# Optimization experiments

Measured on AMD Instinct MI355X. Metric: run time of the kernel, lower is better.

The kernel has to match this reference:

```python
import jax, jax.numpy as jnp
import numpy as np

DIM = 1024
NUM_HEADS = 16
B, T = 2, 2048


def setup_inputs() -> dict:
    key = jax.random.key(0)
    ks = jax.random.split(key, 7)
    s = 0.02
    return {
        "Q": jax.random.normal(ks[0], (B, T, DIM), dtype=jnp.float32),
        "K": jax.random.normal(ks[1], (B, T, DIM), dtype=jnp.float32),
        "V": jax.random.normal(ks[2], (B, T, DIM), dtype=jnp.float32),
        "Wq": jax.random.normal(ks[3], (DIM, DIM), dtype=jnp.float32) * s,
        "Wk": jax.random.normal(ks[4], (DIM, DIM), dtype=jnp.float32) * s,
        "Wv": jax.random.normal(ks[5], (DIM, DIM), dtype=jnp.float32) * s,
        "Wp": jax.random.normal(ks[6], (DIM, DIM), dtype=jnp.float32) * s,
    }


def _split_heads(x, h):
    b, t, d = x.shape
    return x.reshape(b, t, h, d // h).transpose(0, 2, 1, 3)  # b h t d


def reference(Q, K, V, Wq, Wk, Wv, Wp):
    b, t, d = Q.shape
    h = NUM_HEADS
    # NOTE: module scales by 1/sqrt(dim) (full model dim), not 1/sqrt(head_dim)
    scale = 1.0 / np.sqrt(d).astype(np.float32)
    # torch Linear: x @ W.T (bias=False)
    q = _split_heads(Q @ Wq.T, h)  # b h t hd
    k = _split_heads(K @ Wk.T, h)
    v = _split_heads(V @ Wv.T, h)
    att = jnp.einsum('bhid,bhjd->bhij', q, k) * scale  # b h t t
    causal = jnp.tril(jnp.ones((t, t), dtype=bool))
    att = jnp.where(causal[None, None], att, -jnp.inf)
    att = jax.nn.softmax(att, axis=-1)
    y = jnp.einsum('bhij,bhjd->bhid', att, v)  # b h t hd
    y = y.transpose(0, 2, 1, 3).reshape(b, t, d)
    y = y @ Wp.T
    return (y, att, k, v)
```

## Files before the change

kernel.cpp:

```cpp
#include <hip/hip_runtime.h>

typedef __attribute__((ext_vector_type(8))) short s16x8;
typedef __attribute__((ext_vector_type(4))) float f32x4;

static __device__ __forceinline__ unsigned short f2bf(float f) {
  union { float f; unsigned int u; } v; v.f = f;
  unsigned int u = v.u;
  u += 0x7fffu + ((u >> 16) & 1u);
  return (unsigned short)(u >> 16);
}
static __device__ __forceinline__ void gload16(const void* g, void* l) {
  __builtin_amdgcn_global_load_lds((const __attribute__((address_space(1))) unsigned int*)g,
                                   (__attribute__((address_space(3))) unsigned int*)l, 16, 0, 0);
}

__global__ __launch_bounds__(256) void cast7_bf16(
    const float* __restrict__ i0, const float* __restrict__ i1, const float* __restrict__ i2,
    const float* __restrict__ i3, const float* __restrict__ i4, const float* __restrict__ i5,
    const float* __restrict__ i6,
    unsigned short* __restrict__ o0, unsigned short* __restrict__ o1,
    unsigned short* __restrict__ o2, unsigned short* __restrict__ o3,
    unsigned short* __restrict__ o4, unsigned short* __restrict__ o5,
    unsigned short* __restrict__ o6) {
  const int z = blockIdx.z;
  const float* in = z == 0 ? i0 : z == 1 ? i1 : z == 2 ? i2 : z == 3 ? i3 : z == 4 ? i4
                    : z == 5 ? i5 : i6;
  unsigned short* out = z == 0 ? o0 : z == 1 ? o1 : z == 2 ? o2 : z == 3 ? o3 : z == 4 ? o4
                        : z == 5 ? o5 : o6;
  const int n = (z < 3) ? 4194304 : 1048576;
  int i = (blockIdx.x * 256 + threadIdx.x) * 8;
  if (i >= n) return;
  float4 a = *reinterpret_cast<const float4*>(in + i);
  float4 b = *reinterpret_cast<const float4*>(in + i + 4);
  s16x8 o;
  o[0] = (short)f2bf(a.x); o[1] = (short)f2bf(a.y);
  o[2] = (short)f2bf(a.z); o[3] = (short)f2bf(a.w);
  o[4] = (short)f2bf(b.x); o[5] = (short)f2bf(b.y);
  o[6] = (short)f2bf(b.z); o[7] = (short)f2bf(b.w);
  *reinterpret_cast<s16x8*>(out + i) = o;
}

__global__ __launch_bounds__(256) void gemm_bf16(
    const unsigned short* __restrict__ A0, const unsigned short* __restrict__ A1,
    const unsigned short* __restrict__ A2,
    const unsigned short* __restrict__ W0, const unsigned short* __restrict__ W1,
    const unsigned short* __restrict__ W2,
    unsigned short* __restrict__ Oq, unsigned short* __restrict__ Ok,
    float* __restrict__ Kf, unsigned short* __restrict__ OvT,
    float* __restrict__ Vf) {
  __shared__ __align__(16) char LDS[32768];

  const int z = blockIdx.z;
  const unsigned short* A = z == 0 ? A0 : z == 1 ? A1 : A2;
  const unsigned short* W = z == 0 ? W0 : z == 1 ? W1 : W2;

  const int tid = threadIdx.x, lane = tid & 63, w = tid >> 6;
  const int wm = w >> 1, wn = w & 1;
  const int row0 = blockIdx.y * 128, col0 = blockIdx.x * 128;

  f32x4 acc[4][4];
#pragma unroll
  for (int m = 0; m < 4; ++m)
#pragma unroll
    for (int n = 0; n < 4; ++n) acc[m][n] = f32x4{0.f, 0.f, 0.f, 0.f};

  const int srow = tid >> 3;
  const int swb = ((tid & 7) * 16) ^ ((srow & 7) << 4);
  const unsigned short* aSrc = A + (size_t)(row0 + srow) * 1024 + (swb >> 1);
  const unsigned short* bSrc = W + (size_t)(col0 + srow) * 1024 + (swb >> 1);
  char* ldsA = LDS + w * 1024;
  char* ldsB = LDS + 16384 + w * 1024;

  const int lr = lane & 15, g16 = (lane >> 4) * 16;

  for (int k0 = 0; k0 < 1024; k0 += 64) {
    __syncthreads();
#pragma unroll
    for (int p = 0; p < 4; ++p) gload16(aSrc + (size_t)p * 32 * 1024 + k0, ldsA + p * 4096);
#pragma unroll
    for (int p = 0; p < 4; ++p) gload16(bSrc + (size_t)p * 32 * 1024 + k0, ldsB + p * 4096);
    __syncthreads();

    s16x8 af[2][4], bf[2][4];
#pragma unroll
    for (int ks = 0; ks < 2; ++ks) {
#pragma unroll
      for (int m = 0; m < 4; ++m) {
        int r = wm * 64 + m * 16 + lr;
        int cb = (ks * 64 + g16) ^ ((r & 7) << 4);
        af[ks][m] = *reinterpret_cast<const s16x8*>(LDS + r * 128 + cb);
      }
#pragma unroll
      for (int n = 0; n < 4; ++n) {
        int r = wn * 64 + n * 16 + lr;
        int cb = (ks * 64 + g16) ^ ((r & 7) << 4);
        bf[ks][n] = *reinterpret_cast<const s16x8*>(LDS + 16384 + r * 128 + cb);
      }
    }
#pragma unroll
    for (int ks = 0; ks < 2; ++ks)
#pragma unroll
      for (int m = 0; m < 4; ++m)
#pragma unroll
        for (int n = 0; n < 4; ++n)
          acc[m][n] = __builtin_amdgcn_mfma_f32_16x16x32_bf16(af[ks][m], bf[ks][n], acc[m][n], 0, 0, 0);
  }

  const int er = (lane >> 4) * 4, ec = lane & 15;
  const int b = row0 >> 11, trow = row0 & 2047;

  {
    float* F = (z == 1) ? Kf : (z == 2) ? Vf : nullptr;
    if (F) {
#pragma unroll
      for (int m = 0; m < 4; ++m)
#pragma unroll
        for (int n = 0; n < 4; ++n)
#pragma unroll
          for (int j = 0; j < 4; ++j) {
            int t = trow + wm * 64 + m * 16 + er + j;
            int gd = col0 + wn * 64 + n * 16 + ec;
            F[((size_t)(b * 16 + (gd >> 6)) * 2048 + t) * 64 + (gd & 63)] = acc[m][n][j];
          }
    }
  }

  __syncthreads();
  if (z == 2) {
#pragma unroll
    for (int m = 0; m < 4; ++m)
#pragma unroll
      for (int n = 0; n < 4; ++n)
#pragma unroll
        for (int j = 0; j < 4; ++j) {
          int d = wn * 64 + n * 16 + ec, t = wm * 64 + m * 16 + er + j;
          *reinterpret_cast<short*>(LDS + d * 256 + t * 2) = (short)f2bf(acc[m][n][j]);
        }
    __syncthreads();
    const int dr = tid >> 1, half = tid & 1;
    const int gd = col0 + dr, h = gd >> 6, dd = gd & 63;
    unsigned short* dst = OvT + ((size_t)(b * 16 + h) * 64 + dd) * 2048 + trow + half * 64;
    const char* src = LDS + dr * 256 + half * 128;
#pragma unroll
    for (int i = 0; i < 8; ++i)
      *reinterpret_cast<s16x8*>(dst + i * 8) = *reinterpret_cast<const s16x8*>(src + i * 16);
  } else {
    unsigned short* On = (z == 0) ? Oq : Ok;
#pragma unroll
    for (int m = 0; m < 4; ++m)
#pragma unroll
      for (int n = 0; n < 4; ++n)
#pragma unroll
        for (int j = 0; j < 4; ++j) {
          int r = wm * 64 + m * 16 + er + j, c = wn * 64 + n * 16 + ec;
          *reinterpret_cast<short*>(LDS + r * 256 + c * 2) = (short)f2bf(acc[m][n][j]);
        }
    __syncthreads();
    const int r = tid >> 1, half = tid & 1;
    const int h = (col0 >> 6) + half;
    unsigned short* dst = On + ((size_t)(b * 16 + h) * 2048 + trow + r) * 64;
    const char* src = LDS + r * 256 + half * 128;
#pragma unroll
    for (int i = 0; i < 8; ++i)
      *reinterpret_cast<s16x8*>(dst + i * 8) = *reinterpret_cast<const s16x8*>(src + i * 16);
  }
}

__global__ __launch_bounds__(256) void gemm_proj64(
    const unsigned short* __restrict__ A, const unsigned short* __restrict__ W,
    float* __restrict__ Orm) {
  __shared__ __align__(16) char LDS[24576];

  const int tid = threadIdx.x, lane = tid & 63, w = tid >> 6;
  const int row0 = blockIdx.y * 64, col0 = blockIdx.x * 128;

  f32x4 acc[4][2];
#pragma unroll
  for (int m = 0; m < 4; ++m)
#pragma unroll
    for (int n = 0; n < 2; ++n) acc[m][n] = f32x4{0.f, 0.f, 0.f, 0.f};

  const int srow = tid >> 3;
  const int swb = ((tid & 7) * 16) ^ ((srow & 7) << 4);
  const unsigned short* aSrc = A + (size_t)(row0 + srow) * 1024 + (swb >> 1);
  const unsigned short* bSrc = W + (size_t)(col0 + srow) * 1024 + (swb >> 1);
  char* ldsA = LDS + w * 1024;
  char* ldsB = LDS + 8192 + w * 1024;

  const int lr = lane & 15, g16 = (lane >> 4) * 16;

  for (int k0 = 0; k0 < 1024; k0 += 64) {
    __syncthreads();
#pragma unroll
    for (int p = 0; p < 2; ++p) gload16(aSrc + (size_t)p * 32 * 1024 + k0, ldsA + p * 4096);
#pragma unroll
    for (int p = 0; p < 4; ++p) gload16(bSrc + (size_t)p * 32 * 1024 + k0, ldsB + p * 4096);
    __syncthreads();

    s16x8 af[2][4], bf[2][2];
#pragma unroll
    for (int ks = 0; ks < 2; ++ks) {
#pragma unroll
      for (int m = 0; m < 4; ++m) {
        int r = m * 16 + lr;
        int cb = (ks * 64 + g16) ^ ((r & 7) << 4);
        af[ks][m] = *reinterpret_cast<const s16x8*>(LDS + r * 128 + cb);
      }
#pragma unroll
      for (int n = 0; n < 2; ++n) {
        int r = w * 32 + n * 16 + lr;
        int cb = (ks * 64 + g16) ^ ((r & 7) << 4);
        bf[ks][n] = *reinterpret_cast<const s16x8*>(LDS + 8192 + r * 128 + cb);
      }
    }
#pragma unroll
    for (int ks = 0; ks < 2; ++ks)
#pragma unroll
      for (int m = 0; m < 4; ++m)
#pragma unroll
        for (int n = 0; n < 2; ++n)
          acc[m][n] = __builtin_amdgcn_mfma_f32_16x16x32_bf16(af[ks][m], bf[ks][n], acc[m][n], 0, 0, 0);
  }

  const int er = (lane >> 4) * 4, ec = lane & 15;
#pragma unroll
  for (int m = 0; m < 4; ++m)
#pragma unroll
    for (int n = 0; n < 2; ++n)
#pragma unroll
      for (int j = 0; j < 4; ++j)
        Orm[(size_t)(row0 + m * 16 + er + j) * 1024 + col0 + w * 32 + n * 16 + ec] = acc[m][n][j];
}

#define ALD 68

__global__ __launch_bounds__(256) void attn_kernel(
    const unsigned short* __restrict__ qw, const unsigned short* __restrict__ kw,
    const unsigned short* __restrict__ vt, float* __restrict__ att_out,
    unsigned short* __restrict__ yb) {
  __shared__ __align__(16) char LDSA[2][16384];
  __shared__ short Pl[4][16 * ALD];

  const int tid = threadIdx.x, lane = tid & 63, w = tid >> 6;
  const int flat = blockIdx.y * 32 + blockIdx.x;
  const int xcd = flat & 7, idx = flat >> 3;
  const int bh = xcd * 4 + (idx >> 5);
  const int iblk = 31 - (idx & 31);
  const float scale2 = 0.03125f * 1.44269504f;

  const int lr = lane & 15, g16 = (lane >> 4) * 16;
  const int lk = (lane >> 4) * 8, er = (lane >> 4) * 4;
  const int rbase = iblk * 64 + w * 16 + er;

  s16x8 aq[2];
  {
    const unsigned short* qb = qw + ((size_t)bh * 2048 + iblk * 64 + w * 16 + lr) * 64;
    aq[0] = *reinterpret_cast<const s16x8*>(qb + lk);
    aq[1] = *reinterpret_cast<const s16x8*>(qb + 32 + lk);
  }

  const int sw = ((lane & 7) * 16) ^ ((lane >> 3) << 4);
  const unsigned short* kLane = kw + (size_t)bh * 131072 + (size_t)(lane >> 3) * 64 + (sw >> 1);
  const unsigned short* vLane = vt + (size_t)bh * 131072 + (size_t)(lane >> 3) * 2048 + (sw >> 1);

  float lrow[4] = {0.f, 0.f, 0.f, 0.f};

  {
    const int npairs = (iblk + 2) >> 1;
#pragma unroll
    for (int i = 0; i < 4; ++i)
      gload16(kLane + (size_t)(w * 32 + i * 8) * 64, LDSA[0] + w * 4096 + i * 1024);
    __syncthreads();
    int buf = 0;
    for (int p = 0; p < npairs; ++p) {
      if (p + 1 < npairs) {
#pragma unroll
        for (int i = 0; i < 4; ++i)
          gload16(kLane + (size_t)((p + 1) * 128 + w * 32 + i * 8) * 64,
                  LDSA[buf ^ 1] + w * 4096 + i * 1024);
      }
#pragma unroll
      for (int sub = 0; sub < 2; ++sub) {
        int jt = 2 * p + sub;
        if (jt > iblk) break;
        const char* Kb = LDSA[buf] + sub * 8192;
        f32x4 s[4];
#pragma unroll
        for (int n = 0; n < 4; ++n) {
          s[n] = f32x4{0.f, 0.f, 0.f, 0.f};
          int r = n * 16 + lr;
#pragma unroll
          for (int ks = 0; ks < 2; ++ks) {
            int cb = (ks * 64 + g16) ^ ((r & 7) << 4);
            s16x8 bK = *reinterpret_cast<const s16x8*>(Kb + r * 128 + cb);
            s[n] = __builtin_amdgcn_mfma_f32_16x16x32_bf16(aq[ks], bK, s[n], 0, 0, 0);
          }
        }
#pragma unroll
        for (int n = 0; n < 4; ++n) {
          int c = jt * 64 + n * 16 + lr;
#pragma unroll
          for (int j = 0; j < 4; ++j) {
            float sv = (c > rbase + j) ? -1e30f : s[n][j] * scale2;
            s[n][j] = __builtin_exp2f(sv);
          }
        }
#pragma unroll
        for (int j = 0; j < 4; ++j)
          lrow[j] += (s[0][j] + s[1][j]) + (s[2][j] + s[3][j]);
      }
      __syncthreads();
      buf ^= 1;
    }
  }

  float rl[4];
#pragma unroll
  for (int j = 0; j < 4; ++j) {
#pragma unroll
    for (int msk = 1; msk < 16; msk <<= 1) lrow[j] += __shfl_xor(lrow[j], msk);
    rl[j] = 1.0f / lrow[j];
  }

  f32x4 yacc[4];
#pragma unroll
  for (int n = 0; n < 4; ++n) yacc[n] = f32x4{0.f, 0.f, 0.f, 0.f};

  {
    gload16(kLane + (size_t)(w * 8) * 64, LDSA[0] + w * 1024);
    gload16(kLane + (size_t)(w * 8 + 32) * 64, LDSA[0] + w * 1024 + 4096);
    gload16(vLane + (size_t)(w * 8) * 2048, LDSA[0] + 8192 + w * 1024);
    gload16(vLane + (size_t)(w * 8 + 32) * 2048, LDSA[0] + 8192 + w * 1024 + 4096);
    __syncthreads();
    int buf = 0;
    for (int jt = 0; jt <= iblk; ++jt) {
      if (jt < iblk) {
        gload16(kLane + (size_t)((jt + 1) * 64 + w * 8) * 64, LDSA[buf ^ 1] + w * 1024);
        gload16(kLane + (size_t)((jt + 1) * 64 + w * 8 + 32) * 64, LDSA[buf ^ 1] + w * 1024 + 4096);
        gload16(vLane + (size_t)(w * 8) * 2048 + (jt + 1) * 64, LDSA[buf ^ 1] + 8192 + w * 1024);
        gload16(vLane + (size_t)(w * 8 + 32) * 2048 + (jt + 1) * 64,
                LDSA[buf ^ 1] + 8192 + w * 1024 + 4096);
      }
      f32x4 s[4];
#pragma unroll
      for (int n = 0; n < 4; ++n) {
        s[n] = f32x4{0.f, 0.f, 0.f, 0.f};
        int r = n * 16 + lr;
#pragma unroll
        for (int ks = 0; ks < 2; ++ks) {
          int cb = (ks * 64 + g16) ^ ((r & 7) << 4);
          s16x8 bK = *reinterpret_cast<const s16x8*>(LDSA[buf] + r * 128 + cb);
          s[n] = __builtin_amdgcn_mfma_f32_16x16x32_bf16(aq[ks], bK, s[n], 0, 0, 0);
        }
      }
#pragma unroll
      for (int n = 0; n < 4; ++n) {
        int c = jt * 64 + n * 16 + lr;
#pragma unroll
        for (int j = 0; j < 4; ++j) {
          float sv = (c > rbase + j) ? -1e30f : s[n][j] * scale2;
          float p = __builtin_exp2f(sv) * rl[j];
          att_out[((size_t)bh * 2048 + rbase + j) * 2048 + c] = p;
          Pl[w][(er + j) * ALD + n * 16 + lr] = (short)f2bf(p);
        }
      }
#pragma unroll
      for (int ks = 0; ks < 2; ++ks) {
        s16x8 ap = *reinterpret_cast<const s16x8*>(&Pl[w][lr * ALD + ks * 32 + lk]);
#pragma unroll
        for (int n = 0; n < 4; ++n) {
          int r = n * 16 + lr;
          int cb = (ks * 64 + g16) ^ ((r & 7) << 4);
          s16x8 bv = *reinterpret_cast<const s16x8*>(LDSA[buf] + 8192 + r * 128 + cb);
          yacc[n] = __builtin_amdgcn_mfma_f32_16x16x32_bf16(ap, bv, yacc[n], 0, 0, 0);
        }
      }
      asm volatile("s_waitcnt vmcnt(16)" ::: "memory");
      __builtin_amdgcn_s_barrier();
      __builtin_amdgcn_sched_barrier(0);
      buf ^= 1;
    }
  }

  const int b = bh >> 4, h = bh & 15;
#pragma unroll
  for (int n = 0; n < 4; ++n)
#pragma unroll
    for (int j = 0; j < 4; ++j)
      Pl[w][(er + j) * ALD + n * 16 + lr] = (short)f2bf(yacc[n][j]);
  {
    const int yr = lane >> 2, ch = lane & 3;
    s16x8 v0 = *reinterpret_cast<const s16x8*>(&Pl[w][yr * ALD + ch * 16]);
    s16x8 v1 = *reinterpret_cast<const s16x8*>(&Pl[w][yr * ALD + ch * 16 + 8]);
    unsigned short* dst = yb + ((size_t)b * 2048 + iblk * 64 + w * 16 + yr) * 1024 + h * 64 + ch * 16;
    *reinterpret_cast<s16x8*>(dst) = v0;
    *reinterpret_cast<s16x8*>(dst + 8) = v1;
  }

  int c0 = (iblk + 1) * 64;
  if (c0 < 2048) {
    int nv = (2048 - c0) >> 2;
    const float4 z4 = make_float4(0.f, 0.f, 0.f, 0.f);
    for (int rr = 0; rr < 64; rr += 4) {
      int r = rr + w;
      float4* dst = reinterpret_cast<float4*>(att_out + ((size_t)bh * 2048 + iblk * 64 + r) * 2048 + c0);
      for (int i = lane; i < nv; i += 64) dst[i] = z4;
    }
  }
}

extern "C" void kernel_launch(void* const* d_in, const int* in_sizes, int n_in,
                              void* d_out, int out_size, void* d_ws, size_t ws_size,
                              hipStream_t stream) {
  (void)in_sizes; (void)n_in; (void)out_size; (void)ws_size;
  const float* Q = (const float*)d_in[0];
  const float* K = (const float*)d_in[1];
  const float* V = (const float*)d_in[2];
  const float* Wq = (const float*)d_in[3];
  const float* Wk = (const float*)d_in[4];
  const float* Wv = (const float*)d_in[5];
  const float* Wp = (const float*)d_in[6];
  float* out = (float*)d_out;

  char* ws = (char*)d_ws;
  const size_t MB = 1024 * 1024;
  unsigned short* qb = (unsigned short*)(ws + 0 * MB);
  unsigned short* kb = (unsigned short*)(ws + 8 * MB);
  unsigned short* vb = (unsigned short*)(ws + 16 * MB);
  unsigned short* wqb = (unsigned short*)(ws + 24 * MB);
  unsigned short* wkb = (unsigned short*)(ws + 26 * MB);
  unsigned short* wvb = (unsigned short*)(ws + 28 * MB);
  unsigned short* wpb = (unsigned short*)(ws + 30 * MB);
  unsigned short* qws = (unsigned short*)(ws + 32 * MB);
  unsigned short* kws = (unsigned short*)(ws + 40 * MB);
  unsigned short* vwt = (unsigned short*)(ws + 48 * MB);
  unsigned short* yb = (unsigned short*)(ws + 0 * MB);

  float* att_out = out + 4194304;
  float* k_out = out + 138412032;
  float* v_out = out + 142606336;

  cast7_bf16<<<dim3(2048, 1, 7), 256, 0, stream>>>(Q, K, V, Wq, Wk, Wv, Wp,
                                                   qb, kb, vb, wqb, wkb, wvb, wpb);

  gemm_bf16<<<dim3(8, 32, 3), 256, 0, stream>>>(qb, kb, vb, wqb, wkb, wvb,
                                                qws, kws, k_out, vwt, v_out);

  attn_kernel<<<dim3(32, 32), 256, 0, stream>>>(qws, kws, vwt, att_out, yb);

  gemm_proj64<<<dim3(8, 64), 256, 0, stream>>>(yb, wpb, out);
}
```

Before: 247.9 us.

## Split attention into separate row-statistics and probability-write kernels

The fused attention kernel becomes two kernels. The first computes the softmax row sums, stores their reciprocals in a workspace buffer and zero-fills the upper-triangular part of the attention output. The second reloads those reciprocals, recomputes scores, writes normalized probabilities and accumulates P·V. This may help register pressure and occupancy in each kernel, and it moves the zero-fill stores into the lighter stats pass, at the cost of an extra launch and a small global round trip for the row statistics.

Measured after the change: 296.5 us. 1.2x slower.

```diff
diff --git a/kernel.cpp b/kernel.cpp
--- a/kernel.cpp
+++ b/kernel.cpp
@@ -232,14 +232,10 @@
         Orm[(size_t)(row0 + m * 16 + er + j) * 1024 + col0 + w * 32 + n * 16 + ec] = acc[m][n][j];
 }
 
-#define ALD 68
-
-__global__ __launch_bounds__(256) void attn_kernel(
+__global__ __launch_bounds__(256) void attn_stats(
     const unsigned short* __restrict__ qw, const unsigned short* __restrict__ kw,
-    const unsigned short* __restrict__ vt, float* __restrict__ att_out,
-    unsigned short* __restrict__ yb) {
+    float* __restrict__ rl_ws, float* __restrict__ att_out) {
   __shared__ __align__(16) char LDSA[2][16384];
-  __shared__ short Pl[4][16 * ALD];
 
   const int tid = threadIdx.x, lane = tid & 63, w = tid >> 6;
   const int flat = blockIdx.y * 32 + blockIdx.x;
@@ -261,7 +257,6 @@
 
   const int sw = ((lane & 7) * 16) ^ ((lane >> 3) << 4);
   const unsigned short* kLane = kw + (size_t)bh * 131072 + (size_t)(lane >> 3) * 64 + (sw >> 1);
-  const unsigned short* vLane = vt + (size_t)bh * 131072 + (size_t)(lane >> 3) * 2048 + (sw >> 1);
 
   float lrow[4] = {0.f, 0.f, 0.f, 0.f};
 
@@ -314,13 +309,63 @@
     }
   }
 
+#pragma unroll
+  for (int j = 0; j < 4; ++j) {
+#pragma unroll
+    for (int msk = 1; msk < 16; msk <<= 1) lrow[j] += __shfl_xor(lrow[j], msk);
+  }
+  if ((lane & 15) == 0) {
+#pragma unroll
+    for (int j = 0; j < 4; ++j)
+      rl_ws[(size_t)bh * 2048 + rbase + j] = 1.0f / lrow[j];
+  }
+
+  int c0 = (iblk + 1) * 64;
+  if (c0 < 2048) {
+    int nv = (2048 - c0) >> 2;
+    const float4 z4 = make_float4(0.f, 0.f, 0.f, 0.f);
+    for (int rr = 0; rr < 64; rr += 4) {
+      int r = rr + w;
+      float4* dst = reinterpret_cast<float4*>(att_out + ((size_t)bh * 2048 + iblk * 64 + r) * 2048 + c0);
+      for (int i = lane; i < nv; i += 64) dst[i] = z4;
+    }
+  }
+}
+
+#define ALD 68
+
+__global__ __launch_bounds__(256) void attn_write(
+    const unsigned short* __restrict__ qw, const unsigned short* __restrict__ kw,
+    const unsigned short* __restrict__ vt, const float* __restrict__ rl_ws,
+    float* __restrict__ att_out, unsigned short* __restrict__ yb) {
+  __shared__ __align__(16) char LDSA[2][16384];
+  __shared__ short Pl[4][16 * ALD];
+
+  const int tid = threadIdx.x, lane = tid & 63, w = tid >> 6;
+  const int flat = blockIdx.y * 32 + blockIdx.x;
+  const int xcd = flat & 7, idx = flat >> 3;
+  const int bh = xcd * 4 + (idx >> 5);
+  const int iblk = 31 - (idx & 31);
+  const float scale2 = 0.03125f * 1.44269504f;
+
+  const int lr = lane & 15, g16 = (lane >> 4) * 16;
+  const int lk = (lane >> 4) * 8, er = (lane >> 4) * 4;
+  const int rbase = iblk * 64 + w * 16 + er;
+
+  s16x8 aq[2];
+  {
+    const unsigned short* qb = qw + ((size_t)bh * 2048 + iblk * 64 + w * 16 + lr) * 64;
+    aq[0] = *reinterpret_cast<const s16x8*>(qb + lk);
+    aq[1] = *reinterpret_cast<const s16x8*>(qb + 32 + lk);
+  }
+
   float rl[4];
 #pragma unroll
-  for (int j = 0; j < 4; ++j) {
-#pragma unroll
-    for (int msk = 1; msk < 16; msk <<= 1) lrow[j] += __shfl_xor(lrow[j], msk);
-    rl[j] = 1.0f / lrow[j];
-  }
+  for (int j = 0; j < 4; ++j) rl[j] = rl_ws[(size_t)bh * 2048 + rbase + j];
+
+  const int sw = ((lane & 7) * 16) ^ ((lane >> 3) << 4);
+  const unsigned short* kLane = kw + (size_t)bh * 131072 + (size_t)(lane >> 3) * 64 + (sw >> 1);
+  const unsigned short* vLane = vt + (size_t)bh * 131072 + (size_t)(lane >> 3) * 2048 + (sw >> 1);
 
   f32x4 yacc[4];
 #pragma unroll
@@ -395,17 +440,6 @@
     unsigned short* dst = yb + ((size_t)b * 2048 + iblk * 64 + w * 16 + yr) * 1024 + h * 64 + ch * 16;
     *reinterpret_cast<s16x8*>(dst) = v0;
     *reinterpret_cast<s16x8*>(dst + 8) = v1;
-  }
-
-  int c0 = (iblk + 1) * 64;
-  if (c0 < 2048) {
-    int nv = (2048 - c0) >> 2;
-    const float4 z4 = make_float4(0.f, 0.f, 0.f, 0.f);
-    for (int rr = 0; rr < 64; rr += 4) {
-      int r = rr + w;
-      float4* dst = reinterpret_cast<float4*>(att_out + ((size_t)bh * 2048 + iblk * 64 + r) * 2048 + c0);
-      for (int i = lane; i < nv; i += 64) dst[i] = z4;
-    }
   }
 }
 
@@ -434,6 +468,7 @@
   unsigned short* qws = (unsigned short*)(ws + 32 * MB);
   unsigned short* kws = (unsigned short*)(ws + 40 * MB);
   unsigned short* vwt = (unsigned short*)(ws + 48 * MB);
+  float*          rlw = (float*)(ws + 56 * MB);
   unsigned short* yb = (unsigned short*)(ws + 0 * MB);
 
   float* att_out = out + 4194304;
@@ -446,7 +481,9 @@
   gemm_bf16<<<dim3(8, 32, 3), 256, 0, stream>>>(qb, kb, vb, wqb, wkb, wvb,
                                                 qws, kws, k_out, vwt, v_out);
 
-  attn_kernel<<<dim3(32, 32), 256, 0, stream>>>(qws, kws, vwt, att_out, yb);
+  attn_stats<<<dim3(32, 32), 256, 0, stream>>>(qws, kws, rlw, att_out);
+
+  attn_write<<<dim3(32, 32), 256, 0, stream>>>(qws, kws, vwt, rlw, att_out, yb);
 
   gemm_proj64<<<dim3(8, 64), 256, 0, stream>>>(yb, wpb, out);
 }
```
